# Kernel optimization log

Measured on AMD Instinct MI355X. Metric: run time of the kernel, lower is better.

The kernel has to match this reference:

```python
import jax, jax.numpy as jnp
import numpy as np

L, B, H, P = 2048, 16, 512, 256
EPS = 1e-6  # flax nnx LayerNorm default


def setup_inputs() -> dict:
    key = jax.random.key(0)
    ks = jax.random.split(key, 12)
    x = jax.random.normal(ks[0], (L, B, H), jnp.float32)
    d = jax.random.bernoulli(ks[1], 0.01, (L, B))  # sparse reset signal
    hidden_re = jnp.zeros((1, B, P), jnp.float32)
    hidden_im = jnp.zeros((1, B, P), jnp.float32)
    # S5 diagonal state matrix (stable: Re < 0)
    Lambda_re = -0.5 * jnp.exp(0.5 * jax.random.normal(ks[2], (P,), jnp.float32))
    Lambda_im = np.float32(np.pi) * jax.random.normal(ks[3], (P,), jnp.float32)
    B_re = jax.random.normal(ks[4], (P, H), jnp.float32) / np.sqrt(2.0 * H).astype(np.float32)
    B_im = jax.random.normal(ks[5], (P, H), jnp.float32) / np.sqrt(2.0 * H).astype(np.float32)
    C_re = jax.random.normal(ks[6], (H, P), jnp.float32) / np.sqrt(P).astype(np.float32)
    C_im = jax.random.normal(ks[7], (H, P), jnp.float32) / np.sqrt(P).astype(np.float32)
    D = jax.random.normal(ks[8], (H,), jnp.float32)
    log_step = jax.random.uniform(ks[9], (P,), jnp.float32,
                                  minval=np.log(1e-3).astype(np.float32),
                                  maxval=np.log(1e-1).astype(np.float32))
    ln_scale = jnp.ones((H,), jnp.float32)
    ln_bias = jnp.zeros((H,), jnp.float32)
    out2_w = jax.random.normal(ks[10], (H, H), jnp.float32) / np.sqrt(H).astype(np.float32)
    out2_b = jnp.zeros((H,), jnp.float32)
    return dict(x=x, d=d, hidden_re=hidden_re, hidden_im=hidden_im,
                Lambda_re=Lambda_re, Lambda_im=Lambda_im, B_re=B_re, B_im=B_im,
                C_re=C_re, C_im=C_im, D=D, log_step=log_step,
                ln_scale=ln_scale, ln_bias=ln_bias, out2_w=out2_w, out2_b=out2_b)


def reference(x, d, hidden_re, hidden_im, Lambda_re, Lambda_im, B_re, B_im,
              C_re, C_im, D, log_step, ln_scale, ln_bias, out2_w, out2_b):
    def ln(v):
        mu = v.mean(-1, keepdims=True)
        var = v.var(-1, keepdims=True)
        return (v - mu) * jax.lax.rsqrt(var + EPS) * ln_scale + ln_bias

    skip = x
    xn = ln(x)  # prenorm

    # --- S5 SSM (ZOH discretization), vmapped over batch == vectorized over axis 1 ---
    step = jnp.exp(log_step)  # step_rescale = 1.0
    Lam = (Lambda_re + 1j * Lambda_im).astype(jnp.complex64)          # (P,)
    Lam_bar = jnp.exp(Lam * step.astype(jnp.complex64))                # (P,)
    B_bar = ((Lam_bar - 1.0) / Lam)[:, None] * (B_re + 1j * B_im).astype(jnp.complex64)  # (P,H)
    Bu = jnp.einsum('lbh,ph->lbp', xn.astype(jnp.complex64), B_bar)    # (L,B,P)

    keep = (1.0 - d.astype(jnp.float32)).astype(jnp.complex64)         # reset zeroes the carry
    a = Lam_bar[None, None, :] * keep[:, :, None]                      # (L,B,P)
    h0 = (hidden_re + 1j * hidden_im).astype(jnp.complex64)[0]         # (B,P)
    Bu = Bu.at[0].add(a[0] * h0)                                       # fold in initial hidden

    def binop(e1, e2):
        a1, b1 = e1
        a2, b2 = e2
        return (a2 * a1, a2 * b1 + b2)

    _, xs = jax.lax.associative_scan(binop, (a, Bu), axis=0)           # (L,B,P) states
    Cmat = (C_re + 1j * C_im).astype(jnp.complex64)
    ys = 2.0 * jnp.einsum('lbp,hp->lbh', xs, Cmat).real + D * xn       # conj-sym readout + feedthrough
    new_hidden = xs[-1:]                                               # (1,B,P)

    y = ln(ys)  # gtrxl norm (shared LayerNorm)
    # half_glu2: x * sigmoid(W2 gelu(x) + b2)
    x1 = jax.nn.gelu(y)  # approximate=True matches nnx.gelu
    y = y * jax.nn.sigmoid(x1 @ out2_w + out2_b)
    out = skip + y
    return (new_hidden.real, new_hidden.imag, out)
```

## Files before the change

### kernel.cpp

```cpp
#include <hip/hip_runtime.h>

#define LL 2048
#define BB 16
#define HH 512
#define PP 256
#define MM (LL*BB)
#define NN 512
#define KK 512
#define NC 64
#define CLEN 32
#define NKT (KK/64)

typedef __bf16 bf16x8 __attribute__((ext_vector_type(8)));
typedef float  f32x4  __attribute__((ext_vector_type(4)));

__device__ __forceinline__ unsigned short f2bf(float f) {
  unsigned u = __builtin_bit_cast(unsigned, f);
  u = (u + 0x7fffu + ((u >> 16) & 1u)) >> 16;
  return (unsigned short)u;
}
__device__ __forceinline__ float bf2f(unsigned short s) {
  unsigned u = ((unsigned)s) << 16;
  return __builtin_bit_cast(float, u);
}

__global__ void detect_kernel(const unsigned int* __restrict__ dw, int* __restrict__ flag) {
  __shared__ int sInt, sFloat;
  if (threadIdx.x == 0) { sInt = 1; sFloat = 1; }
  __syncthreads();
  int allInt = 1, allFloat = 1;
  for (int i = threadIdx.x; i < 8192; i += 256) {
    unsigned v = dw[i];
    if (v > 1u) allInt = 0;
    if (v != 0u && v != 0x3f800000u) allFloat = 0;
  }
  if (!allInt) atomicAnd(&sInt, 0);
  if (!allFloat) atomicAnd(&sFloat, 0);
  __syncthreads();
  if (threadIdx.x == 0) *flag = sInt ? 0 : (sFloat ? 1 : 2);
}

__device__ __forceinline__ float keep_val(const void* d, int flag, int idx) {
  if (flag == 0) return 1.f - (float)((const int*)d)[idx];
  if (flag == 1) return 1.f - ((const float*)d)[idx];
  return 1.f - (float)((const unsigned char*)d)[idx];
}

__global__ void precompute_kernel(
    const float* __restrict__ Lre, const float* __restrict__ Lim,
    const float* __restrict__ Bre, const float* __restrict__ Bim,
    const float* __restrict__ Cre, const float* __restrict__ Cim,
    const float* __restrict__ lstep, const float* __restrict__ w2,
    unsigned short* __restrict__ W1t, unsigned short* __restrict__ W2t,
    unsigned short* __restrict__ W3t, float* __restrict__ lam_re,
    float* __restrict__ lam_im) {
  int t = blockIdx.x * 256 + threadIdx.x;
  int k = t & (KK - 1);
  int n = t >> 9;
  {
    int p = n & (PP - 1);
    float lr = Lre[p], li = Lim[p];
    float st = expf(lstep[p]);
    float er = expf(lr * st);
    float ang = li * st;
    float lbr = er * cosf(ang), lbi = er * sinf(ang);
    float den = lr * lr + li * li;
    float wr = ((lbr - 1.f) * lr + lbi * li) / den;
    float wi = (lbi * lr - (lbr - 1.f) * li) / den;
    float br = Bre[p * HH + k], bi = Bim[p * HH + k];
    float v = (n < PP) ? (wr * br - wi * bi) : (wr * bi + wi * br);
    W1t[(size_t)n * KK + k] = f2bf(v);
  }
  {
    float v = (k < PP) ? (2.f * Cre[n * PP + k]) : (-2.f * Cim[n * PP + (k - PP)]);
    W2t[(size_t)n * KK + k] = f2bf(v);
  }
  W3t[(size_t)n * KK + k] = f2bf(w2[(size_t)k * HH + n]);
  if (t < PP) {
    float lr = Lre[t], li = Lim[t];
    float st = expf(lstep[t]);
    float er = expf(lr * st);
    float ang = li * st;
    lam_re[t] = er * cosf(ang);
    lam_im[t] = er * sinf(ang);
  }
}

__global__ void ln1_kernel(const float* __restrict__ x, const float* __restrict__ sc,
                           const float* __restrict__ bs, unsigned short* __restrict__ xn) {
  int row = blockIdx.x * 4 + (threadIdx.x >> 6);
  int lane = threadIdx.x & 63;
  const float4* xr = (const float4*)(x + (size_t)row * HH) + lane * 2;
  float4 a = xr[0], b = xr[1];
  float s = (a.x + a.y) + (a.z + a.w) + (b.x + b.y) + (b.z + b.w);
  float q = a.x * a.x + a.y * a.y + a.z * a.z + a.w * a.w +
            b.x * b.x + b.y * b.y + b.z * b.z + b.w * b.w;
#pragma unroll
  for (int off = 32; off; off >>= 1) { s += __shfl_xor(s, off); q += __shfl_xor(q, off); }
  float mean = s * (1.f / HH);
  float var = fmaxf(q * (1.f / HH) - mean * mean, 0.f);
  float rstd = rsqrtf(var + 1e-6f);
  const float4* scp = (const float4*)sc + lane * 2;
  const float4* bsp = (const float4*)bs + lane * 2;
  float4 s0 = scp[0], s1 = scp[1], b0 = bsp[0], b1 = bsp[1];
  unsigned short o[8];
  o[0] = f2bf((a.x - mean) * rstd * s0.x + b0.x);
  o[1] = f2bf((a.y - mean) * rstd * s0.y + b0.y);
  o[2] = f2bf((a.z - mean) * rstd * s0.z + b0.z);
  o[3] = f2bf((a.w - mean) * rstd * s0.w + b0.w);
  o[4] = f2bf((b.x - mean) * rstd * s1.x + b1.x);
  o[5] = f2bf((b.y - mean) * rstd * s1.y + b1.y);
  o[6] = f2bf((b.z - mean) * rstd * s1.z + b1.z);
  o[7] = f2bf((b.w - mean) * rstd * s1.w + b1.w);
  uint4 pk;
  pk.x = o[0] | ((unsigned)o[1] << 16);
  pk.y = o[2] | ((unsigned)o[3] << 16);
  pk.z = o[4] | ((unsigned)o[5] << 16);
  pk.w = o[6] | ((unsigned)o[7] << 16);
  *((uint4*)(xn + (size_t)row * HH) + lane) = pk;
}

__global__ void ln2_kernel(const unsigned short* __restrict__ ys, const float* __restrict__ sc,
                           const float* __restrict__ bs, unsigned short* __restrict__ y,
                           unsigned short* __restrict__ x1) {
  int row = blockIdx.x * 4 + (threadIdx.x >> 6);
  int lane = threadIdx.x & 63;
  uint4 pin = *((const uint4*)(ys + (size_t)row * HH) + lane);
  float v[8];
  v[0] = bf2f((unsigned short)(pin.x & 0xffff)); v[1] = bf2f((unsigned short)(pin.x >> 16));
  v[2] = bf2f((unsigned short)(pin.y & 0xffff)); v[3] = bf2f((unsigned short)(pin.y >> 16));
  v[4] = bf2f((unsigned short)(pin.z & 0xffff)); v[5] = bf2f((unsigned short)(pin.z >> 16));
  v[6] = bf2f((unsigned short)(pin.w & 0xffff)); v[7] = bf2f((unsigned short)(pin.w >> 16));
  float s = 0.f, q = 0.f;
#pragma unroll
  for (int j = 0; j < 8; j++) { s += v[j]; q += v[j] * v[j]; }
#pragma unroll
  for (int off = 32; off; off >>= 1) { s += __shfl_xor(s, off); q += __shfl_xor(q, off); }
  float mean = s * (1.f / HH);
  float var = fmaxf(q * (1.f / HH) - mean * mean, 0.f);
  float rstd = rsqrtf(var + 1e-6f);
  const float4* scp = (const float4*)sc + lane * 2;
  const float4* bsp = (const float4*)bs + lane * 2;
  float4 s0 = scp[0], s1 = scp[1], b0 = bsp[0], b1 = bsp[1];
  float scv[8] = { s0.x, s0.y, s0.z, s0.w, s1.x, s1.y, s1.z, s1.w };
  float bsv[8] = { b0.x, b0.y, b0.z, b0.w, b1.x, b1.y, b1.z, b1.w };
  unsigned short oy[8], og[8];
#pragma unroll
  for (int j = 0; j < 8; j++) {
    float yv = (v[j] - mean) * rstd * scv[j] + bsv[j];
    oy[j] = f2bf(yv);
    float g = 0.5f * yv * (1.f + tanhf(0.7978845608f * (yv + 0.044715f * yv * yv * yv)));
    og[j] = f2bf(g);
  }
  uint4 py, pg;
  py.x = oy[0] | ((unsigned)oy[1] << 16); py.y = oy[2] | ((unsigned)oy[3] << 16);
  py.z = oy[4] | ((unsigned)oy[5] << 16); py.w = oy[6] | ((unsigned)oy[7] << 16);
  pg.x = og[0] | ((unsigned)og[1] << 16); pg.y = og[2] | ((unsigned)og[3] << 16);
  pg.z = og[4] | ((unsigned)og[5] << 16); pg.w = og[6] | ((unsigned)og[7] << 16);
  *((uint4*)(y  + (size_t)row * HH) + lane) = py;
  *((uint4*)(x1 + (size_t)row * HH) + lane) = pg;
}

template <int EPI>
__global__ __launch_bounds__(256, 2) void gemm_kernel(
    const unsigned short* __restrict__ A, const unsigned short* __restrict__ Wt,
    void* __restrict__ Cout, const float* __restrict__ Dvec,
    const unsigned short* __restrict__ aux16, const float* __restrict__ skip) {
  __shared__ alignas(16) unsigned short lA[2][128 * 64];
  __shared__ alignas(16) unsigned short lB[2][128 * 64];
  int tid = threadIdx.x;
  int w = tid >> 6, lane = tid & 63;
  int wgid = blockIdx.x;
  int xcd = wgid & 7, bidx = wgid >> 3;
  int m0 = (xcd * 32 + (bidx >> 2)) * 128;
  int n0 = (bidx & 3) * 128;
  int wr = w >> 1, wc = w & 1;
  f32x4 acc[4][4];
#pragma unroll
  for (int i = 0; i < 4; i++)
#pragma unroll
    for (int j = 0; j < 4; j++) acc[i][j] = (f32x4){0.f, 0.f, 0.f, 0.f};

  auto stage = [&](int buf, int kt) {
#pragma unroll
    for (int i = 0; i < 4; i++) {
      int sidx = i * 256 + tid;
      int r = sidx >> 3, c = sidx & 7;
      int cs = c ^ (r & 7);
      const unsigned short* g = A + (size_t)(m0 + r) * KK + kt * 64 + cs * 8;
      unsigned short* l = &lA[buf][(i * 256 + w * 64) * 8];
      __builtin_amdgcn_global_load_lds((const __attribute__((address_space(1))) void*)g,
                                       (__attribute__((address_space(3))) void*)l, 16, 0, 0);
    }
#pragma unroll
    for (int i = 0; i < 4; i++) {
      int sidx = i * 256 + tid;
      int r = sidx >> 3, c = sidx & 7;
      int cs = c ^ (r & 7);
      const unsigned short* g = Wt + (size_t)(n0 + r) * KK + kt * 64 + cs * 8;
      unsigned short* l = &lB[buf][(i * 256 + w * 64) * 8];
      __builtin_amdgcn_global_load_lds((const __attribute__((address_space(1))) void*)g,
                                       (__attribute__((address_space(3))) void*)l, 16, 0, 0);
    }
  };

  stage(0, 0);
  __syncthreads();
#pragma unroll
  for (int kt = 0; kt < NKT; ++kt) {
    int cur = kt & 1;
    if (kt + 1 < NKT) stage(cur ^ 1, kt + 1);
#pragma unroll
    for (int ks = 0; ks < 2; ++ks) {
      bf16x8 aF[4], bF[4];
#pragma unroll
      for (int m = 0; m < 4; m++) {
        int row = wr * 64 + m * 16 + (lane & 15);
        int s = ks * 4 + (lane >> 4);
        aF[m] = *reinterpret_cast<const bf16x8*>(&lA[cur][row * 64 + (s ^ (row & 7)) * 8]);
      }
#pragma unroll
      for (int n = 0; n < 4; n++) {
        int row = wc * 64 + n * 16 + (lane & 15);
        int s = ks * 4 + (lane >> 4);
        bF[n] = *reinterpret_cast<const bf16x8*>(&lB[cur][row * 64 + (s ^ (row & 7)) * 8]);
      }
#pragma unroll
      for (int m = 0; m < 4; m++)
#pragma unroll
        for (int n = 0; n < 4; n++)
          acc[m][n] = __builtin_amdgcn_mfma_f32_16x16x32_bf16(aF[m], bF[n], acc[m][n], 0, 0, 0);
    }
    __syncthreads();
  }
  int lr4 = (lane >> 4) * 4, lc = lane & 15;
#pragma unroll
  for (int m = 0; m < 4; m++) {
    int rowb = m0 + wr * 64 + m * 16 + lr4;
#pragma unroll
    for (int n = 0; n < 4; n++) {
      int col = n0 + wc * 64 + n * 16 + lc;
#pragma unroll
      for (int j = 0; j < 4; j++) {
        int row = rowb + j;
        size_t idxo = (size_t)row * NN + col;
        float v = acc[m][n][j];
        if (EPI == 0) {
          ((unsigned short*)Cout)[idxo] = f2bf(v);
        } else if (EPI == 1) {
          ((unsigned short*)Cout)[idxo] = f2bf(v + Dvec[col] * bf2f(aux16[idxo]));
        } else {
          float z = v + Dvec[col];
          float sg = 1.f / (1.f + expf(-z));
          ((float*)Cout)[idxo] = skip[idxo] + bf2f(aux16[idxo]) * sg;
        }
      }
    }
  }
}

__global__ void scanA_kernel(const unsigned short* __restrict__ Bu, const void* __restrict__ d,
                             const int* __restrict__ dflag, const float* __restrict__ lam_re,
                             const float* __restrict__ lam_im, float* __restrict__ Ar,
                             float* __restrict__ Ai, float* __restrict__ Sr,
                             float* __restrict__ Si) {
  int bx = blockIdx.x;
  int c = bx >> 4, b = bx & 15;
  int p = threadIdx.x;
  int fl = *dflag;
  float lr = lam_re[p], li = lam_im[p];
  float Apr = 1.f, Api = 0.f, sr = 0.f, si = 0.f;
  int l0 = c * CLEN;
  for (int j = 0; j < CLEN; j++) {
    int l = l0 + j;
    float kp = keep_val(d, fl, l * BB + b);
    float ar = lr * kp, ai = li * kp;
    size_t ro = (size_t)(l * BB + b) * NN;
    float bur = bf2f(Bu[ro + p]), bui = bf2f(Bu[ro + PP + p]);
    float nsr = ar * sr - ai * si + bur;
    float nsi = ar * si + ai * sr + bui;
    sr = nsr; si = nsi;
    float nar = ar * Apr - ai * Api;
    float nai = ar * Api + ai * Apr;
    Apr = nar; Api = nai;
  }
  int o = bx * PP + p;
  Ar[o] = Apr; Ai[o] = Api; Sr[o] = sr; Si[o] = si;
}

__global__ void scanB_kernel(const float* __restrict__ hr0, const float* __restrict__ hi0,
                             const float* __restrict__ Ar, const float* __restrict__ Ai,
                             const float* __restrict__ Sr, const float* __restrict__ Si,
                             float* __restrict__ Cr, float* __restrict__ Ci,
                             float* __restrict__ outHid) {
  int b = blockIdx.x;
  int p = threadIdx.x;
  float cr = hr0[b * PP + p], ci = hi0[b * PP + p];
  for (int c = 0; c < NC; c++) {
    int o = (c * BB + b) * PP + p;
    Cr[o] = cr; Ci[o] = ci;
    float ar = Ar[o], ai = Ai[o];
    float nr = ar * cr - ai * ci + Sr[o];
    float ni = ar * ci + ai * cr + Si[o];
    cr = nr; ci = ni;
  }
  outHid[b * PP + p] = cr;
  outHid[BB * PP + b * PP + p] = ci;
}

__global__ void scanC_kernel(const unsigned short* __restrict__ Bu, const void* __restrict__ d,
                             const int* __restrict__ dflag, const float* __restrict__ lam_re,
                             const float* __restrict__ lam_im, const float* __restrict__ Cr,
                             const float* __restrict__ Ci, unsigned short* __restrict__ xs) {
  int bx = blockIdx.x;
  int c = bx >> 4, b = bx & 15;
  int p = threadIdx.x;
  int fl = *dflag;
  float lr = lam_re[p], li = lam_im[p];
  float hr = Cr[bx * PP + p], hi = Ci[bx * PP + p];
  int l0 = c * CLEN;
  for (int j = 0; j < CLEN; j++) {
    int l = l0 + j;
    float kp = keep_val(d, fl, l * BB + b);
    float ar = lr * kp, ai = li * kp;
    size_t ro = (size_t)(l * BB + b) * NN;
    float bur = bf2f(Bu[ro + p]), bui = bf2f(Bu[ro + PP + p]);
    float nhr = ar * hr - ai * hi + bur;
    float nhi = ar * hi + ai * hr + bui;
    hr = nhr; hi = nhi;
    xs[ro + p] = f2bf(hr);
    xs[ro + PP + p] = f2bf(hi);
  }
}

extern "C" void kernel_launch(void* const* d_in, const int* in_sizes, int n_in,
                              void* d_out, int out_size, void* d_ws, size_t ws_size,
                              hipStream_t stream) {
  const float* x    = (const float*)d_in[0];
  const void*  dmask= d_in[1];
  const float* hidr = (const float*)d_in[2];
  const float* hidi = (const float*)d_in[3];
  const float* Lre  = (const float*)d_in[4];
  const float* Lim  = (const float*)d_in[5];
  const float* Bre  = (const float*)d_in[6];
  const float* Bim  = (const float*)d_in[7];
  const float* Cre  = (const float*)d_in[8];
  const float* Cim  = (const float*)d_in[9];
  const float* Dv   = (const float*)d_in[10];
  const float* lst  = (const float*)d_in[11];
  const float* lsc  = (const float*)d_in[12];
  const float* lbs  = (const float*)d_in[13];
  const float* w2   = (const float*)d_in[14];
  const float* b2   = (const float*)d_in[15];
  float* out = (float*)d_out;

  char* ws = (char*)d_ws;
  size_t off = 0;
  auto alloc = [&](size_t bytes) -> void* {
    void* p = ws + off;
    off += (bytes + 255) & ~(size_t)255;
    return p;
  };
  unsigned short* xn  = (unsigned short*)alloc((size_t)MM * KK * 2);
  unsigned short* xs  = (unsigned short*)alloc((size_t)MM * KK * 2);
  unsigned short* Bu  = (unsigned short*)alloc((size_t)MM * NN * 2);
  unsigned short* W1t = (unsigned short*)alloc((size_t)NN * KK * 2);
  unsigned short* W2t = (unsigned short*)alloc((size_t)NN * KK * 2);
  unsigned short* W3t = (unsigned short*)alloc((size_t)NN * KK * 2);
  float* lam_re = (float*)alloc(PP * 4);
  float* lam_im = (float*)alloc(PP * 4);
  float* Ar = (float*)alloc((size_t)NC * BB * PP * 4);
  float* Ai = (float*)alloc((size_t)NC * BB * PP * 4);
  float* Sr = (float*)alloc((size_t)NC * BB * PP * 4);
  float* Si = (float*)alloc((size_t)NC * BB * PP * 4);
  float* Cr = (float*)alloc((size_t)NC * BB * PP * 4);
  float* Ci = (float*)alloc((size_t)NC * BB * PP * 4);
  int* dflag = (int*)alloc(256);
  unsigned short* y   = xn;
  unsigned short* x1  = xs;
  unsigned short* ysb = Bu;

  detect_kernel<<<1, 256, 0, stream>>>((const unsigned int*)dmask, dflag);
  precompute_kernel<<<1024, 256, 0, stream>>>(Lre, Lim, Bre, Bim, Cre, Cim, lst, w2,
                                              W1t, W2t, W3t, lam_re, lam_im);
  ln1_kernel<<<MM / 4, 256, 0, stream>>>(x, lsc, lbs, xn);
  gemm_kernel<0><<<1024, 256, 0, stream>>>(xn, W1t, Bu, nullptr, nullptr, nullptr);
  scanA_kernel<<<NC * BB, 256, 0, stream>>>(Bu, dmask, dflag, lam_re, lam_im, Ar, Ai, Sr, Si);
  scanB_kernel<<<BB, 256, 0, stream>>>(hidr, hidi, Ar, Ai, Sr, Si, Cr, Ci, out);
  scanC_kernel<<<NC * BB, 256, 0, stream>>>(Bu, dmask, dflag, lam_re, lam_im, Cr, Ci, xs);
  gemm_kernel<1><<<1024, 256, 0, stream>>>(xs, W2t, ysb, Dv, xn, nullptr);
  ln2_kernel<<<MM / 4, 256, 0, stream>>>(ysb, lsc, lbs, y, x1);
  gemm_kernel<2><<<1024, 256, 0, stream>>>(x1, W3t, out + 2 * BB * PP, b2, y, x);
}
```

Baseline: 196.2 us.

## Rewrite GEMM with 512-thread blocks, deeper LDS pipeline, and LDS-staged coalesced epilogue

Replaces the 256-thread double-buffered GEMM with a 512-thread, 8-wave kernel. It uses a K-step of 32 and a multi-buffer LDS ring (4 A buffers, 3 B buffers), waits on explicit vmcnt counts, and raises wave priority around the MFMA block so loads overlap compute. The epilogue now stages each output chunk through LDS so global stores (and the aux/skip reads) are vectorized and coalesced instead of scattered scalar stores. This adds more barriers per K iteration and in the epilogue, and the hand-tuned waitcnt counts are fragile.

```diff
diff --git a/kernel.cpp b/kernel.cpp
--- a/kernel.cpp
+++ b/kernel.cpp
@@ -9,7 +9,6 @@
 #define KK 512
 #define NC 64
 #define CLEN 32
-#define NKT (KK/64)
 
 typedef __bf16 bf16x8 __attribute__((ext_vector_type(8)));
 typedef float  f32x4  __attribute__((ext_vector_type(4)));
@@ -162,99 +161,146 @@
 }
 
 template <int EPI>
-__global__ __launch_bounds__(256, 2) void gemm_kernel(
+__global__ __launch_bounds__(512, 4) void gemmP_kernel(
     const unsigned short* __restrict__ A, const unsigned short* __restrict__ Wt,
     void* __restrict__ Cout, const float* __restrict__ Dvec,
     const unsigned short* __restrict__ aux16, const float* __restrict__ skip) {
-  __shared__ alignas(16) unsigned short lA[2][128 * 64];
-  __shared__ alignas(16) unsigned short lB[2][128 * 64];
-  int tid = threadIdx.x;
-  int w = tid >> 6, lane = tid & 63;
-  int wgid = blockIdx.x;
-  int xcd = wgid & 7, bidx = wgid >> 3;
-  int m0 = (xcd * 32 + (bidx >> 2)) * 128;
-  int n0 = (bidx & 3) * 128;
-  int wr = w >> 1, wc = w & 1;
-  f32x4 acc[4][4];
+  __shared__ char lds[57344];
+  unsigned short* lA = (unsigned short*)lds;
+  unsigned short* lB = (unsigned short*)(lds + 32768);
+  const int tid = threadIdx.x;
+  const int w = tid >> 6, lane = tid & 63;
+  const int wr = w >> 2, wc = w & 3;
+  const int l15 = lane & 15, g16 = lane >> 4;
+  const int wgid = blockIdx.x;
+  const int xcd = wgid & 7, bidx = wgid >> 3;
+  const int m0 = (xcd * 32 + (bidx >> 2)) * 128;
+  const int n0 = (bidx & 3) * 128;
+
+  const int sRow = tid >> 2;
+  const int sC = (tid & 3) ^ (sRow & 3);
+  const unsigned short* aSrc = A + (size_t)(m0 + sRow) * KK + sC * 8;
+  const unsigned short* bSrc = Wt + (size_t)(n0 + sRow) * KK + sC * 8;
+
+  auto sA = [&](int buf, int kt) {
+    __builtin_amdgcn_global_load_lds(
+        (const __attribute__((address_space(1))) void*)(aSrc + kt * 32),
+        (__attribute__((address_space(3))) void*)(lA + buf * 4096 + (w * 64) * 8), 16, 0, 0);
+  };
+  auto sB = [&](int buf, int kt) {
+    __builtin_amdgcn_global_load_lds(
+        (const __attribute__((address_space(1))) void*)(bSrc + kt * 32),
+        (__attribute__((address_space(3))) void*)(lB + buf * 4096 + (w * 64) * 8), 16, 0, 0);
+  };
+  auto rdA = [&](int buf, int fm) -> bf16x8 {
+    int row = wr * 64 + fm * 16 + l15;
+    return *(const bf16x8*)(lA + buf * 4096 + row * 32 + (g16 ^ (row & 3)) * 8);
+  };
+  auto rdB = [&](int buf, int fn) -> bf16x8 {
+    int row = wc * 32 + fn * 16 + l15;
+    return *(const bf16x8*)(lB + buf * 4096 + row * 32 + (g16 ^ (row & 3)) * 8);
+  };
+
+  f32x4 acc[4][2];
 #pragma unroll
   for (int i = 0; i < 4; i++)
 #pragma unroll
-    for (int j = 0; j < 4; j++) acc[i][j] = (f32x4){0.f, 0.f, 0.f, 0.f};
-
-  auto stage = [&](int buf, int kt) {
-#pragma unroll
-    for (int i = 0; i < 4; i++) {
-      int sidx = i * 256 + tid;
-      int r = sidx >> 3, c = sidx & 7;
-      int cs = c ^ (r & 7);
-      const unsigned short* g = A + (size_t)(m0 + r) * KK + kt * 64 + cs * 8;
-      unsigned short* l = &lA[buf][(i * 256 + w * 64) * 8];
-      __builtin_amdgcn_global_load_lds((const __attribute__((address_space(1))) void*)g,
-                                       (__attribute__((address_space(3))) void*)l, 16, 0, 0);
-    }
-#pragma unroll
-    for (int i = 0; i < 4; i++) {
-      int sidx = i * 256 + tid;
-      int r = sidx >> 3, c = sidx & 7;
-      int cs = c ^ (r & 7);
-      const unsigned short* g = Wt + (size_t)(n0 + r) * KK + kt * 64 + cs * 8;
-      unsigned short* l = &lB[buf][(i * 256 + w * 64) * 8];
-      __builtin_amdgcn_global_load_lds((const __attribute__((address_space(1))) void*)g,
-                                       (__attribute__((address_space(3))) void*)l, 16, 0, 0);
-    }
-  };
-
-  stage(0, 0);
-  __syncthreads();
-#pragma unroll
-  for (int kt = 0; kt < NKT; ++kt) {
-    int cur = kt & 1;
-    if (kt + 1 < NKT) stage(cur ^ 1, kt + 1);
-#pragma unroll
-    for (int ks = 0; ks < 2; ++ks) {
-      bf16x8 aF[4], bF[4];
-#pragma unroll
-      for (int m = 0; m < 4; m++) {
-        int row = wr * 64 + m * 16 + (lane & 15);
-        int s = ks * 4 + (lane >> 4);
-        aF[m] = *reinterpret_cast<const bf16x8*>(&lA[cur][row * 64 + (s ^ (row & 7)) * 8]);
-      }
-#pragma unroll
-      for (int n = 0; n < 4; n++) {
-        int row = wc * 64 + n * 16 + (lane & 15);
-        int s = ks * 4 + (lane >> 4);
-        bF[n] = *reinterpret_cast<const bf16x8*>(&lB[cur][row * 64 + (s ^ (row & 7)) * 8]);
-      }
-#pragma unroll
-      for (int m = 0; m < 4; m++)
-#pragma unroll
-        for (int n = 0; n < 4; n++)
-          acc[m][n] = __builtin_amdgcn_mfma_f32_16x16x32_bf16(aF[m], bF[n], acc[m][n], 0, 0, 0);
-    }
-    __syncthreads();
-  }
-  int lr4 = (lane >> 4) * 4, lc = lane & 15;
-#pragma unroll
-  for (int m = 0; m < 4; m++) {
-    int rowb = m0 + wr * 64 + m * 16 + lr4;
-#pragma unroll
-    for (int n = 0; n < 4; n++) {
-      int col = n0 + wc * 64 + n * 16 + lc;
-#pragma unroll
-      for (int j = 0; j < 4; j++) {
-        int row = rowb + j;
-        size_t idxo = (size_t)row * NN + col;
-        float v = acc[m][n][j];
-        if (EPI == 0) {
-          ((unsigned short*)Cout)[idxo] = f2bf(v);
-        } else if (EPI == 1) {
-          ((unsigned short*)Cout)[idxo] = f2bf(v + Dvec[col] * bf2f(aux16[idxo]));
-        } else {
-          float z = v + Dvec[col];
-          float sg = 1.f / (1.f + expf(-z));
-          ((float*)Cout)[idxo] = skip[idxo] + bf2f(aux16[idxo]) * sg;
+    for (int j = 0; j < 2; j++) acc[i][j] = (f32x4){0.f, 0.f, 0.f, 0.f};
+
+  sB(0, 0); sA(0, 0); sB(1, 1); sA(1, 1); sA(2, 2);
+  asm volatile("s_waitcnt vmcnt(3)" ::: "memory");
+  __builtin_amdgcn_s_barrier();
+
+#pragma unroll
+  for (int k = 0; k < 16; ++k) {
+    bf16x8 aF[4], bF[2];
+#pragma unroll
+    for (int fm = 0; fm < 4; fm++) aF[fm] = rdA(k & 3, fm);
+#pragma unroll
+    for (int fn = 0; fn < 2; fn++) bF[fn] = rdB(k % 3, fn);
+    if (k + 2 < 16) sB((k + 2) % 3, k + 2);
+    if (k + 3 < 16) sA((k + 3) & 3, k + 3);
+    asm volatile("s_waitcnt lgkmcnt(0)" ::: "memory");
+    __builtin_amdgcn_sched_barrier(0);
+    __builtin_amdgcn_s_setprio(1);
+#pragma unroll
+    for (int fm = 0; fm < 4; fm++)
+#pragma unroll
+      for (int fn = 0; fn < 2; fn++)
+        acc[fm][fn] = __builtin_amdgcn_mfma_f32_16x16x32_bf16(aF[fm], bF[fn], acc[fm][fn], 0, 0, 0);
+    __builtin_amdgcn_s_setprio(0);
+    if (k <= 12)      asm volatile("s_waitcnt vmcnt(3)" ::: "memory");
+    else if (k == 13) asm volatile("s_waitcnt vmcnt(2)" ::: "memory");
+    else              asm volatile("s_waitcnt vmcnt(0)" ::: "memory");
+    __builtin_amdgcn_s_barrier();
+  }
+
+  if (EPI == 0 || EPI == 1) {
+    unsigned short* lbf = (unsigned short*)lds;
+#pragma unroll
+    for (int ch = 0; ch < 8; ++ch) {
+      if (wr == (ch >> 2)) {
+        int fm = ch & 3;
+#pragma unroll
+        for (int fn = 0; fn < 2; fn++) {
+          int col = wc * 32 + fn * 16 + l15;
+#pragma unroll
+          for (int jj = 0; jj < 4; jj++)
+            lbf[(g16 * 4 + jj) * 136 + col] = f2bf(acc[fm][fn][jj]);
         }
       }
+      __syncthreads();
+      {
+        int r = tid >> 5, tc = tid & 31;
+        int grow = m0 + ch * 16 + r;
+        int gcol = n0 + tc * 4;
+        ushort4 v = *(const ushort4*)&lbf[r * 136 + tc * 4];
+        if (EPI == 0) {
+          *(ushort4*)(((unsigned short*)Cout) + (size_t)grow * NN + gcol) = v;
+        } else {
+          ushort4 au = *(const ushort4*)(aux16 + (size_t)grow * NN + gcol);
+          float4 d = *(const float4*)&Dvec[gcol];
+          ushort4 o;
+          o.x = f2bf(bf2f(v.x) + d.x * bf2f(au.x));
+          o.y = f2bf(bf2f(v.y) + d.y * bf2f(au.y));
+          o.z = f2bf(bf2f(v.z) + d.z * bf2f(au.z));
+          o.w = f2bf(bf2f(v.w) + d.w * bf2f(au.w));
+          *(ushort4*)(((unsigned short*)Cout) + (size_t)grow * NN + gcol) = o;
+        }
+      }
+      __syncthreads();
+    }
+  } else {
+    float* lf = (float*)lds;
+#pragma unroll
+    for (int ch = 0; ch < 8; ++ch) {
+      if (wr == (ch >> 2)) {
+        int fm = ch & 3;
+#pragma unroll
+        for (int fn = 0; fn < 2; fn++) {
+          int col = wc * 32 + fn * 16 + l15;
+#pragma unroll
+          for (int jj = 0; jj < 4; jj++)
+            lf[(g16 * 4 + jj) * 132 + col] = acc[fm][fn][jj];
+        }
+      }
+      __syncthreads();
+      {
+        int r = tid >> 5, tc = tid & 31;
+        int grow = m0 + ch * 16 + r;
+        int gcol = n0 + tc * 4;
+        float4 v = *(const float4*)&lf[r * 132 + tc * 4];
+        float4 d = *(const float4*)&Dvec[gcol];
+        float4 sk = *(const float4*)(skip + (size_t)grow * NN + gcol);
+        ushort4 au = *(const ushort4*)(aux16 + (size_t)grow * NN + gcol);
+        float4 o;
+        o.x = sk.x + bf2f(au.x) / (1.f + expf(-(v.x + d.x)));
+        o.y = sk.y + bf2f(au.y) / (1.f + expf(-(v.y + d.y)));
+        o.z = sk.z + bf2f(au.z) / (1.f + expf(-(v.z + d.z)));
+        o.w = sk.w + bf2f(au.w) / (1.f + expf(-(v.w + d.w)));
+        *(float4*)(((float*)Cout) + (size_t)grow * NN + gcol) = o;
+      }
+      __syncthreads();
     }
   }
 }
@@ -384,11 +430,11 @@
   precompute_kernel<<<1024, 256, 0, stream>>>(Lre, Lim, Bre, Bim, Cre, Cim, lst, w2,
                                               W1t, W2t, W3t, lam_re, lam_im);
   ln1_kernel<<<MM / 4, 256, 0, stream>>>(x, lsc, lbs, xn);
-  gemm_kernel<0><<<1024, 256, 0, stream>>>(xn, W1t, Bu, nullptr, nullptr, nullptr);
+  gemmP_kernel<0><<<1024, 512, 0, stream>>>(xn, W1t, Bu, nullptr, nullptr, nullptr);
   scanA_kernel<<<NC * BB, 256, 0, stream>>>(Bu, dmask, dflag, lam_re, lam_im, Ar, Ai, Sr, Si);
   scanB_kernel<<<BB, 256, 0, stream>>>(hidr, hidi, Ar, Ai, Sr, Si, Cr, Ci, out);
   scanC_kernel<<<NC * BB, 256, 0, stream>>>(Bu, dmask, dflag, lam_re, lam_im, Cr, Ci, xs);
-  gemm_kernel<1><<<1024, 256, 0, stream>>>(xs, W2t, ysb, Dv, xn, nullptr);
+  gemmP_kernel<1><<<1024, 512, 0, stream>>>(xs, W2t, ysb, Dv, xn, nullptr);
   ln2_kernel<<<MM / 4, 256, 0, stream>>>(ysb, lsc, lbs, y, x1);
-  gemm_kernel<2><<<1024, 256, 0, stream>>>(x1, W3t, out + 2 * BB * PP, b2, y, x);
-}
+  gemmP_kernel<2><<<1024, 512, 0, stream>>>(x1, W3t, out + 2 * BB * PP, b2, y, x);
+}
```

New measurement: 196.9 us. No clear change (+0.4%).
